# Kernel tuning notes

Measured on AMD Instinct MI355X. Metric: run time of the kernel, lower is better.

## Reference

```python
import jax, jax.numpy as jnp
import numpy as np
from jax import lax

STATE_LEN = 5
N_BASE = 4
C = N_BASE ** STATE_LEN          # 1024 CRF states
NZ = N_BASE + 1                  # 5 incoming transitions per state
FEAT = 320
KW = 19
STRIDE = 5
SCALE = 5.0


def _transition_idx():
    # bonito CTC_CRF.idx: predecessor state for each (state, transition) pair
    a = np.arange(C)
    idx = np.concatenate([a[:, None], np.repeat(a, N_BASE).reshape(N_BASE, -1).T], axis=1)
    return jnp.asarray(idx, dtype=jnp.int32)  # [C, NZ]


def setup_inputs() -> dict:
    key = jax.random.key(0)
    ks = jax.random.split(key, 5)
    x = jax.random.normal(ks[0], (32, 1, 4000), jnp.float32)
    conv_w = jax.random.normal(ks[1], (FEAT, 1, KW), jnp.float32) * 0.1
    conv_b = jax.random.normal(ks[2], (FEAT,), jnp.float32) * 0.1
    lin_w = jax.random.normal(ks[3], (FEAT, C * NZ), jnp.float32) * (1.0 / np.sqrt(FEAT))
    lin_b = jax.random.normal(ks[4], (C * NZ,), jnp.float32) * 0.1
    return {"x": x, "conv_w": conv_w, "conv_b": conv_b, "lin_w": lin_w, "lin_b": lin_b}


def _encoder(x, conv_w, conv_b, lin_w, lin_b):
    # x: [N, 1, L] -> strided conv -> [N, FEAT, T]
    y = lax.conv_general_dilated(x, conv_w, (STRIDE,), "SAME",
                                 dimension_numbers=("NCH", "OIH", "NCH"))
    y = jnp.tanh(y + conv_b[None, :, None])
    y = jnp.transpose(y, (2, 0, 1))  # [T, N, FEAT]
    # scaled-tanh CRF output head -> [T, N, C*NZ]
    return SCALE * jnp.tanh(jnp.einsum("tnf,fc->tnc", y, lin_w) + lin_b)


def _logZ(scores, idx):
    # log-semiring forward algorithm (alpha_0 = beta_T = 0)
    T, N, _ = scores.shape
    Ms = scores.reshape(T, N, C, NZ)
    alpha0 = jnp.zeros((N, C), scores.dtype)

    def step(alpha, Ms_t):  # Ms_t: [N, C, NZ], alpha: [N, C]
        return jax.nn.logsumexp(Ms_t + alpha[:, idx], axis=2), None

    alpha, _ = lax.scan(step, alpha0, Ms)
    return jax.nn.logsumexp(alpha, axis=1)  # [N]


def reference(x, conv_w, conv_b, lin_w, lin_b):
    idx = _transition_idx()
    scores = _encoder(x, conv_w, conv_b, lin_w, lin_b).astype(jnp.float32)  # [T, N, 5120]
    T = scores.shape[0]
    # GlobalNorm: scores - logZ / T, broadcast over time and channel dims
    return scores - _logZ(scores, idx)[:, None] / T
```

## Files before the change

### kernel.cpp

```cpp
#include <hip/hip_runtime.h>
#include <hip/hip_bf16.h>


typedef __attribute__((ext_vector_type(8))) short bf16x8;
typedef __attribute__((ext_vector_type(4))) float f32x4;

#define T_STEPS 800
#define NBATCH 32
#define FEAT 320
#define CNZ 5120
#define MROWS (T_STEPS * NBATCH)

__device__ __forceinline__ float fast_tanh(float x) {
    float e = exp2f(x * 2.8853900817779268f);
    return 1.0f - 2.0f * __builtin_amdgcn_rcpf(e + 1.0f);
}

__global__ __launch_bounds__(320) void conv_kernel(
    const float* __restrict__ x, const float* __restrict__ w,
    const float* __restrict__ b, __hip_bfloat16* __restrict__ y) {
    int m = blockIdx.x;
    int t = m >> 5, n = m & 31;
    int f = threadIdx.x;
    __shared__ float xs[19];
    int base = t * 5 - 7;
    if (f < 19) {
        int pos = base + f;
        xs[f] = (pos >= 0 && pos < 4000) ? x[n * 4000 + pos] : 0.0f;
    }
    __syncthreads();
    float acc = b[f];
#pragma unroll
    for (int k = 0; k < 19; ++k) acc = fmaf(xs[k], w[f * 19 + k], acc);
    y[(size_t)m * FEAT + f] = __float2bfloat16(fast_tanh(acc));
}

__global__ __launch_bounds__(256) void transpose_w(
    const float* __restrict__ W, __hip_bfloat16* __restrict__ Wt) {
    __shared__ float tile[64][65];
    int nb = blockIdx.x * 64, kb = blockIdx.y * 64;
    int tx = threadIdx.x & 63, ty = threadIdx.x >> 6;
#pragma unroll
    for (int r = 0; r < 64; r += 4)
        tile[ty + r][tx] = W[(size_t)(kb + ty + r) * CNZ + nb + tx];
    __syncthreads();
#pragma unroll
    for (int r = 0; r < 64; r += 4) {
        int nn = ty + r;
        Wt[(size_t)(nb + nn) * FEAT + kb + tx] = __float2bfloat16(tile[tx][nn]);
    }
}

#define GBM 128
#define GBN 128
#define GBK 64
#define LDK 72

__global__ __launch_bounds__(256) void gemm_kernel(
    const __hip_bfloat16* __restrict__ A,
    const __hip_bfloat16* __restrict__ Bt,
    const float* __restrict__ bias,
    float* __restrict__ out) {
    __shared__ __align__(16) short As[GBM * LDK];
    __shared__ __align__(16) short Bs[GBN * LDK];
    const int K = FEAT;
    int bm0 = blockIdx.x * GBM;
    int bn0 = blockIdx.y * GBN;
    int tid = threadIdx.x;
    int wave = tid >> 6, lane = tid & 63;
    int wm = (wave >> 1) * 64, wn = (wave & 1) * 64;
    int col = lane & 15, quad = lane >> 4;

    f32x4 acc[4][4];
#pragma unroll
    for (int i = 0; i < 4; ++i)
#pragma unroll
        for (int j = 0; j < 4; ++j) acc[i][j] = (f32x4){0.f, 0.f, 0.f, 0.f};

    for (int k0 = 0; k0 < K; k0 += GBK) {
#pragma unroll
        for (int p = 0; p < 4; ++p) {
            int i = p * 256 + tid;
            int row = i >> 3, cg = i & 7;
            *(int4*)&As[row * LDK + cg * 8] =
                *(const int4*)&A[(size_t)(bm0 + row) * K + k0 + cg * 8];
            *(int4*)&Bs[row * LDK + cg * 8] =
                *(const int4*)&Bt[(size_t)(bn0 + row) * K + k0 + cg * 8];
        }
        __syncthreads();
#pragma unroll
        for (int kk = 0; kk < GBK; kk += 32) {
            bf16x8 af[4], bfr[4];
#pragma unroll
            for (int i = 0; i < 4; ++i)
                af[i] = *(bf16x8*)&As[(wm + i * 16 + col) * LDK + kk + quad * 8];
#pragma unroll
            for (int j = 0; j < 4; ++j)
                bfr[j] = *(bf16x8*)&Bs[(wn + j * 16 + col) * LDK + kk + quad * 8];
#pragma unroll
            for (int i = 0; i < 4; ++i)
#pragma unroll
                for (int j = 0; j < 4; ++j)
                    acc[i][j] = __builtin_amdgcn_mfma_f32_16x16x32_bf16(
                        af[i], bfr[j], acc[i][j], 0, 0, 0);
        }
        __syncthreads();
    }
#pragma unroll
    for (int j = 0; j < 4; ++j) {
        int n_g = bn0 + wn + j * 16 + col;
        float bj = bias[n_g];
#pragma unroll
        for (int i = 0; i < 4; ++i) {
            int m_base = bm0 + wm + i * 16 + quad * 4;
#pragma unroll
            for (int r = 0; r < 4; ++r) {
                out[(size_t)(m_base + r) * CNZ + n_g] =
                    5.0f * fast_tanh(acc[i][j][r] + bj);
            }
        }
    }
}


__device__ __forceinline__ float lse5_2(float s0, float s1, float s2, float s3,
                                        float s4, float a0, float a1, float a2,
                                        float a3, float a4) {
    const float L2E = 1.4426950408889634f;
    float x0 = fmaf(s0, L2E, a0);
    float x1 = fmaf(s1, L2E, a1);
    float x2 = fmaf(s2, L2E, a2);
    float x3 = fmaf(s3, L2E, a3);
    float x4 = fmaf(s4, L2E, a4);
    float mx = fmaxf(fmaxf(fmaxf(x0, x1), fmaxf(x2, x3)), x4);
    float sum = __builtin_amdgcn_exp2f(x0 - mx) + __builtin_amdgcn_exp2f(x1 - mx) +
                __builtin_amdgcn_exp2f(x2 - mx) + __builtin_amdgcn_exp2f(x3 - mx) +
                __builtin_amdgcn_exp2f(x4 - mx);
    return __builtin_amdgcn_logf(sum) + mx;
}

#define LOADP(P, TT) do {                                                      \
    int tc_ = (TT) < T_STEPS ? (TT) : (T_STEPS - 1);                           \
    const float4* p4_ = (const float4*)(base + (size_t)tc_ * tstride);         \
    P[0] = p4_[0]; P[1] = p4_[1]; P[2] = p4_[2]; P[3] = p4_[3]; P[4] = p4_[4]; \
} while (0)

#define FSTEP(P, TT, cur, nxt) do {                                            \
    float s0_ = P[0].x, s1_ = P[0].y, s2_ = P[0].z, s3_ = P[0].w, s4_ = P[1].x;\
    float t0_ = P[1].y, t1_ = P[1].z, t2_ = P[1].w, t3_ = P[2].x, t4_ = P[2].y;\
    float u0_ = P[2].z, u1_ = P[2].w, u2_ = P[3].x, u3_ = P[3].y, u4_ = P[3].z;\
    float v0_ = P[3].w, v1_ = P[4].x, v2_ = P[4].y, v3_ = P[4].z, v4_ = P[4].w;\
    LOADP(P, TT);                                                              \
    float aq0_ = (cur)[tid], aq1_ = (cur)[tid + 256];                          \
    float aq2_ = (cur)[tid + 512], aq3_ = (cur)[tid + 768];                    \
    float4 ao_ = *(const float4*)&(cur)[4 * tid];                              \
    float4 r_;                                                                 \
    r_.x = lse5_2(s0_, s1_, s2_, s3_, s4_, ao_.x, aq0_, aq1_, aq2_, aq3_);     \
    r_.y = lse5_2(t0_, t1_, t2_, t3_, t4_, ao_.y, aq0_, aq1_, aq2_, aq3_);     \
    r_.z = lse5_2(u0_, u1_, u2_, u3_, u4_, ao_.z, aq0_, aq1_, aq2_, aq3_);     \
    r_.w = lse5_2(v0_, v1_, v2_, v3_, v4_, ao_.w, aq0_, aq1_, aq2_, aq3_);     \
    *(float4*)&(nxt)[4 * tid] = r_;                                            \
    __syncthreads();                                                           \
} while (0)

__global__ __launch_bounds__(256) void forward_kernel(
    const float* __restrict__ scores, float* __restrict__ corr) {
    __shared__ float A0[1024];
    __shared__ float A1[1024];
    const int tid = threadIdx.x;
    const int n = blockIdx.x;
    const float LN2 = 0.6931471805599453f;

    *(float4*)&A0[4 * tid] = (float4){0.f, 0.f, 0.f, 0.f};
    __syncthreads();

    const size_t tstride = (size_t)NBATCH * CNZ;
    const float* base = scores + (size_t)n * CNZ + tid * 20;

    float4 P0[5], P1[5], P2[5], P3[5];
    LOADP(P0, 0); LOADP(P1, 1); LOADP(P2, 2); LOADP(P3, 3);

    for (int t = 0; t < T_STEPS; t += 4) {
        FSTEP(P0, t + 4, A0, A1);
        FSTEP(P1, t + 5, A1, A0);
        FSTEP(P2, t + 6, A0, A1);
        FSTEP(P3, t + 7, A1, A0);
    }
    float4 v = *(const float4*)&A0[4 * tid];
    float pm = fmaxf(fmaxf(v.x, v.y), fmaxf(v.z, v.w));
    A1[tid] = pm;
    __syncthreads();
#pragma unroll
    for (int s = 128; s > 0; s >>= 1) {
        if (tid < s) A1[tid] = fmaxf(A1[tid], A1[tid + s]);
        __syncthreads();
    }
    float mx = A1[0];
    __syncthreads();
    float ps = __builtin_amdgcn_exp2f(v.x - mx) + __builtin_amdgcn_exp2f(v.y - mx) +
               __builtin_amdgcn_exp2f(v.z - mx) + __builtin_amdgcn_exp2f(v.w - mx);
    A1[tid] = ps;
    __syncthreads();
#pragma unroll
    for (int s = 128; s > 0; s >>= 1) {
        if (tid < s) A1[tid] += A1[tid + s];
        __syncthreads();
    }
    if (tid == 0)
        corr[n] = (__builtin_amdgcn_logf(A1[0]) + mx) * LN2 * (1.0f / (float)T_STEPS);
}

__global__ __launch_bounds__(256) void sub_kernel(
    float* __restrict__ out, const float* __restrict__ corr) {
    size_t i4 = (size_t)blockIdx.x * blockDim.x + threadIdx.x;
    float cc = corr[(i4 / (CNZ / 4)) & (NBATCH - 1)];
    float4* o4 = (float4*)out;
    float4 v = o4[i4];
    v.x -= cc; v.y -= cc; v.z -= cc; v.w -= cc;
    o4[i4] = v;
}

extern "C" void kernel_launch(void* const* d_in, const int* in_sizes, int n_in,
                              void* d_out, int out_size, void* d_ws, size_t ws_size,
                              hipStream_t stream) {
    const float* x      = (const float*)d_in[0];
    const float* conv_w = (const float*)d_in[1];
    const float* conv_b = (const float*)d_in[2];
    const float* lin_w  = (const float*)d_in[3];
    const float* lin_b  = (const float*)d_in[4];
    float* out = (float*)d_out;

    char* ws = (char*)d_ws;
    __hip_bfloat16* y  = (__hip_bfloat16*)ws;
    __hip_bfloat16* wt = (__hip_bfloat16*)(ws + 16384000);
    float* corr        = (float*)(ws + 16384000 + 3276800);

    conv_kernel<<<MROWS, 320, 0, stream>>>(x, conv_w, conv_b, y);
    transpose_w<<<dim3(CNZ / 64, FEAT / 64), 256, 0, stream>>>(lin_w, wt);
    gemm_kernel<<<dim3(MROWS / GBM, CNZ / GBN), 256, 0, stream>>>(y, wt, lin_b, out);
    forward_kernel<<<NBATCH, 256, 0, stream>>>(out, corr);
    sub_kernel<<<(out_size / 4) / 256, 256, 0, stream>>>(out, corr);
}
```

Before: 1.432 ms.

## Split CRF recursion into concurrent forward and backward halves with fp16 score copy

Replaces the single serial forward scan with a kernel that runs the forward pass over the first part of time and a backward pass over the rest in separate blocks. A combine kernel then joins alpha and beta to get logZ. This roughly halves the length of the serial dependency chain and doubles the number of busy blocks. The GEMM optionally writes an fp16 copy of the scores so the recursion reads half the bytes, which costs extra write traffic and some precision. The fp16 path is taken only when the workspace is large enough.

```diff
diff --git a/kernel.cpp b/kernel.cpp
--- a/kernel.cpp
+++ b/kernel.cpp
@@ -1,5 +1,7 @@
 #include <hip/hip_runtime.h>
 #include <hip/hip_bf16.h>
+#include <hip/hip_fp16.h>
+#include <type_traits>
 
 
 typedef __attribute__((ext_vector_type(8))) short bf16x8;
@@ -10,6 +12,8 @@
 #define FEAT 320
 #define CNZ 5120
 #define MROWS (T_STEPS * NBATCH)
+#define FSPLIT 480
+#define BSTEPS (T_STEPS - FSPLIT)
 
 __device__ __forceinline__ float fast_tanh(float x) {
     float e = exp2f(x * 2.8853900817779268f);
@@ -60,7 +64,8 @@
     const __hip_bfloat16* __restrict__ A,
     const __hip_bfloat16* __restrict__ Bt,
     const float* __restrict__ bias,
-    float* __restrict__ out) {
+    float* __restrict__ out,
+    __half* __restrict__ s16) {
     __shared__ __align__(16) short As[GBM * LDK];
     __shared__ __align__(16) short Bs[GBN * LDK];
     const int K = FEAT;
@@ -115,8 +120,10 @@
             int m_base = bm0 + wm + i * 16 + quad * 4;
 #pragma unroll
             for (int r = 0; r < 4; ++r) {
-                out[(size_t)(m_base + r) * CNZ + n_g] =
-                    5.0f * fast_tanh(acc[i][j][r] + bj);
+                size_t idx = (size_t)(m_base + r) * CNZ + n_g;
+                float v = 5.0f * fast_tanh(acc[i][j][r] + bj);
+                out[idx] = v;
+                if (s16) s16[idx] = __float2half(v);
             }
         }
     }
@@ -139,75 +146,141 @@
     return __builtin_amdgcn_logf(sum) + mx;
 }
 
-#define LOADP(P, TT) do {                                                      \
-    int tc_ = (TT) < T_STEPS ? (TT) : (T_STEPS - 1);                           \
-    const float4* p4_ = (const float4*)(base + (size_t)tc_ * tstride);         \
-    P[0] = p4_[0]; P[1] = p4_[1]; P[2] = p4_[2]; P[3] = p4_[3]; P[4] = p4_[4]; \
-} while (0)
-
-#define FSTEP(P, TT, cur, nxt) do {                                            \
-    float s0_ = P[0].x, s1_ = P[0].y, s2_ = P[0].z, s3_ = P[0].w, s4_ = P[1].x;\
-    float t0_ = P[1].y, t1_ = P[1].z, t2_ = P[1].w, t3_ = P[2].x, t4_ = P[2].y;\
-    float u0_ = P[2].z, u1_ = P[2].w, u2_ = P[3].x, u3_ = P[3].y, u4_ = P[3].z;\
-    float v0_ = P[3].w, v1_ = P[4].x, v2_ = P[4].y, v3_ = P[4].z, v4_ = P[4].w;\
-    LOADP(P, TT);                                                              \
-    float aq0_ = (cur)[tid], aq1_ = (cur)[tid + 256];                          \
-    float aq2_ = (cur)[tid + 512], aq3_ = (cur)[tid + 768];                    \
-    float4 ao_ = *(const float4*)&(cur)[4 * tid];                              \
-    float4 r_;                                                                 \
-    r_.x = lse5_2(s0_, s1_, s2_, s3_, s4_, ao_.x, aq0_, aq1_, aq2_, aq3_);     \
-    r_.y = lse5_2(t0_, t1_, t2_, t3_, t4_, ao_.y, aq0_, aq1_, aq2_, aq3_);     \
-    r_.z = lse5_2(u0_, u1_, u2_, u3_, u4_, ao_.z, aq0_, aq1_, aq2_, aq3_);     \
-    r_.w = lse5_2(v0_, v1_, v2_, v3_, v4_, ao_.w, aq0_, aq1_, aq2_, aq3_);     \
-    *(float4*)&(nxt)[4 * tid] = r_;                                            \
+__device__ __forceinline__ float cvh(ushort u) { __half h = *(__half*)&u; return __half2float(h); }
+__device__ __forceinline__ float cvh(float f) { return f; }
+
+template<bool FP16>
+__global__ __launch_bounds__(512) void fb_kernel(
+    const void* __restrict__ sc, float* __restrict__ alphaF,
+    float* __restrict__ betaB) {
+    __shared__ __align__(16) float A0[1024];
+    __shared__ __align__(16) float A1[1024];
+    const int tid = threadIdx.x;
+    const int n = blockIdx.x & 31;
+    const int dir = blockIdx.x >> 5;
+
+    *(float2*)&A0[2 * tid] = make_float2(0.f, 0.f);
+    __syncthreads();
+
+    const size_t row = (size_t)NBATCH * CNZ;
+
+    if (dir == 0) {
+        const int q = tid >> 1;
+        const uint* fbu = (const uint*)((const __half*)sc + (size_t)n * CNZ) +
+                          (size_t)tid * 5;
+        const float2* fbf = (const float2*)((const float*)sc + (size_t)n * CNZ +
+                          (size_t)tid * 10);
+
+#define LDF(P, TT) do { int tc_ = (TT) < FSPLIT ? (TT) : (FSPLIT - 1);         \
+    if constexpr (FP16) { const uint* pp_ = fbu + (size_t)tc_ * 81920;         \
+        P[0] = pp_[0]; P[1] = pp_[1]; P[2] = pp_[2]; P[3] = pp_[3]; P[4] = pp_[4]; } \
+    else { const float2* pp_ = fbf + (size_t)tc_ * 81920; float2* d_ = (float2*)P; \
+        d_[0] = pp_[0]; d_[1] = pp_[1]; d_[2] = pp_[2]; d_[3] = pp_[3]; d_[4] = pp_[4]; } \
+} while (0)
+
+#define UNP(P, s) do { if constexpr (FP16) {                                   \
+        float2 f0_ = __half22float2(*(__half2*)&P[0]);                         \
+        float2 f1_ = __half22float2(*(__half2*)&P[1]);                         \
+        float2 f2_ = __half22float2(*(__half2*)&P[2]);                         \
+        float2 f3_ = __half22float2(*(__half2*)&P[3]);                         \
+        float2 f4_ = __half22float2(*(__half2*)&P[4]);                         \
+        s[0]=f0_.x; s[1]=f0_.y; s[2]=f1_.x; s[3]=f1_.y; s[4]=f2_.x;            \
+        s[5]=f2_.y; s[6]=f3_.x; s[7]=f3_.y; s[8]=f4_.x; s[9]=f4_.y; }          \
+    else { const float* f_ = (const float*)P;                                  \
+        s[0]=f_[0]; s[1]=f_[1]; s[2]=f_[2]; s[3]=f_[3]; s[4]=f_[4];            \
+        s[5]=f_[5]; s[6]=f_[6]; s[7]=f_[7]; s[8]=f_[8]; s[9]=f_[9]; }          \
+} while (0)
+
+#define FSTEP(P, TT, cur, nxt) do { float s_[10]; UNP(P, s_); LDF(P, TT);      \
+    float aq0_ = (cur)[q], aq1_ = (cur)[q + 256];                              \
+    float aq2_ = (cur)[q + 512], aq3_ = (cur)[q + 768];                        \
+    float2 ao_ = *(const float2*)&(cur)[2 * tid];                              \
+    float r0_ = lse5_2(s_[0], s_[1], s_[2], s_[3], s_[4], ao_.x, aq0_, aq1_, aq2_, aq3_); \
+    float r1_ = lse5_2(s_[5], s_[6], s_[7], s_[8], s_[9], ao_.y, aq0_, aq1_, aq2_, aq3_); \
+    *(float2*)&(nxt)[2 * tid] = make_float2(r0_, r1_);                         \
     __syncthreads();                                                           \
 } while (0)
 
-__global__ __launch_bounds__(256) void forward_kernel(
-    const float* __restrict__ scores, float* __restrict__ corr) {
-    __shared__ float A0[1024];
-    __shared__ float A1[1024];
-    const int tid = threadIdx.x;
-    const int n = blockIdx.x;
-    const float LN2 = 0.6931471805599453f;
-
-    *(float4*)&A0[4 * tid] = (float4){0.f, 0.f, 0.f, 0.f};
-    __syncthreads();
-
-    const size_t tstride = (size_t)NBATCH * CNZ;
-    const float* base = scores + (size_t)n * CNZ + tid * 20;
-
-    float4 P0[5], P1[5], P2[5], P3[5];
-    LOADP(P0, 0); LOADP(P1, 1); LOADP(P2, 2); LOADP(P3, 3);
-
-    for (int t = 0; t < T_STEPS; t += 4) {
-        FSTEP(P0, t + 4, A0, A1);
-        FSTEP(P1, t + 5, A1, A0);
-        FSTEP(P2, t + 6, A0, A1);
-        FSTEP(P3, t + 7, A1, A0);
-    }
-    float4 v = *(const float4*)&A0[4 * tid];
-    float pm = fmaxf(fmaxf(v.x, v.y), fmaxf(v.z, v.w));
-    A1[tid] = pm;
+        uint P0[10], P1[10], P2[10], P3[10];
+        LDF(P0, 0); LDF(P1, 1); LDF(P2, 2); LDF(P3, 3);
+        for (int t = 0; t < FSPLIT; t += 4) {
+            FSTEP(P0, t + 4, A0, A1);
+            FSTEP(P1, t + 5, A1, A0);
+            FSTEP(P2, t + 6, A0, A1);
+            FSTEP(P3, t + 7, A1, A0);
+        }
+        *(float2*)&alphaF[(size_t)n * 1024 + 2 * tid] = *(const float2*)&A0[2 * tid];
+    } else {
+        using ET = std::conditional_t<FP16, ushort, float>;
+        const int p0 = 2 * tid;
+        const int g = p0 & 255;
+        const int hi = p0 >> 8;
+        const size_t o_self = (size_t)10 * tid;
+        const size_t gb = (size_t)20 * g + 1 + hi;
+        const ET* bb = (const ET*)sc + (size_t)n * CNZ;
+        const int sbase = (8 * tid) & 1023;
+
+#define LDB(E, KK) do { int kc_ = (KK) < BSTEPS ? (KK) : (BSTEPS - 1);         \
+    const ET* pb_ = bb + (size_t)(T_STEPS - 1 - kc_) * row;                    \
+    E[0] = pb_[o_self];      E[1] = pb_[gb];       E[2] = pb_[gb + 5];         \
+    E[3] = pb_[gb + 10];     E[4] = pb_[gb + 15];  E[5] = pb_[o_self + 5];     \
+    E[6] = pb_[gb + 20];     E[7] = pb_[gb + 25];  E[8] = pb_[gb + 30];        \
+    E[9] = pb_[gb + 35];                                                       \
+} while (0)
+
+#define BSTEP(E, KK, cur, nxt) do { float s_[10];                              \
+    s_[0]=cvh(E[0]); s_[1]=cvh(E[1]); s_[2]=cvh(E[2]); s_[3]=cvh(E[3]);        \
+    s_[4]=cvh(E[4]); s_[5]=cvh(E[5]); s_[6]=cvh(E[6]); s_[7]=cvh(E[7]);        \
+    s_[8]=cvh(E[8]); s_[9]=cvh(E[9]); LDB(E, KK);                              \
+    float2 bs_ = *(const float2*)&(cur)[2 * tid];                              \
+    float4 b0_ = *(const float4*)&(cur)[sbase];                                \
+    float4 b1_ = *(const float4*)&(cur)[sbase + 4];                            \
+    float r0_ = lse5_2(s_[0], s_[1], s_[2], s_[3], s_[4], bs_.x, b0_.x, b0_.y, b0_.z, b0_.w); \
+    float r1_ = lse5_2(s_[5], s_[6], s_[7], s_[8], s_[9], bs_.y, b1_.x, b1_.y, b1_.z, b1_.w); \
+    *(float2*)&(nxt)[2 * tid] = make_float2(r0_, r1_);                         \
+    __syncthreads();                                                           \
+} while (0)
+
+        ET E0[10], E1[10], E2[10], E3[10];
+        LDB(E0, 0); LDB(E1, 1); LDB(E2, 2); LDB(E3, 3);
+        for (int k = 0; k < BSTEPS; k += 4) {
+            BSTEP(E0, k + 4, A0, A1);
+            BSTEP(E1, k + 5, A1, A0);
+            BSTEP(E2, k + 6, A0, A1);
+            BSTEP(E3, k + 7, A1, A0);
+        }
+        *(float2*)&betaB[(size_t)n * 1024 + 2 * tid] = *(const float2*)&A0[2 * tid];
+    }
+}
+
+__global__ __launch_bounds__(256) void combine_kernel(
+    const float* __restrict__ aF, const float* __restrict__ bB,
+    float* __restrict__ corr) {
+    __shared__ float R[256];
+    int n = blockIdx.x, tid = threadIdx.x;
+    float4 a = *(const float4*)&aF[(size_t)n * 1024 + 4 * tid];
+    float4 b = *(const float4*)&bB[(size_t)n * 1024 + 4 * tid];
+    float x0 = a.x + b.x, x1 = a.y + b.y, x2 = a.z + b.z, x3 = a.w + b.w;
+    float m = fmaxf(fmaxf(x0, x1), fmaxf(x2, x3));
+    R[tid] = m;
     __syncthreads();
 #pragma unroll
     for (int s = 128; s > 0; s >>= 1) {
-        if (tid < s) A1[tid] = fmaxf(A1[tid], A1[tid + s]);
+        if (tid < s) R[tid] = fmaxf(R[tid], R[tid + s]);
         __syncthreads();
     }
-    float mx = A1[0];
-    __syncthreads();
-    float ps = __builtin_amdgcn_exp2f(v.x - mx) + __builtin_amdgcn_exp2f(v.y - mx) +
-               __builtin_amdgcn_exp2f(v.z - mx) + __builtin_amdgcn_exp2f(v.w - mx);
-    A1[tid] = ps;
+    float mx = R[0];
+    __syncthreads();
+    float sm = exp2f(x0 - mx) + exp2f(x1 - mx) + exp2f(x2 - mx) + exp2f(x3 - mx);
+    R[tid] = sm;
     __syncthreads();
 #pragma unroll
     for (int s = 128; s > 0; s >>= 1) {
-        if (tid < s) A1[tid] += A1[tid + s];
+        if (tid < s) R[tid] += R[tid + s];
         __syncthreads();
     }
     if (tid == 0)
-        corr[n] = (__builtin_amdgcn_logf(A1[0]) + mx) * LN2 * (1.0f / (float)T_STEPS);
+        corr[n] = (log2f(R[0]) + mx) * 0.6931471805599453f * (1.0f / (float)T_STEPS);
 }
 
 __global__ __launch_bounds__(256) void sub_kernel(
@@ -230,14 +303,30 @@
     const float* lin_b  = (const float*)d_in[4];
     float* out = (float*)d_out;
 
+    const size_t Y_OFF    = 0;
+    const size_t WT_OFF   = 16384000;
+    const size_t CORR_OFF = 19660800;
+    const size_t AF_OFF   = 19661056;
+    const size_t BB_OFF   = 19792128;
+    const size_t S16_OFF  = 19923200;
+    const size_t NEED16   = S16_OFF + (size_t)MROWS * CNZ * 2;
+
     char* ws = (char*)d_ws;
-    __hip_bfloat16* y  = (__hip_bfloat16*)ws;
-    __hip_bfloat16* wt = (__hip_bfloat16*)(ws + 16384000);
-    float* corr        = (float*)(ws + 16384000 + 3276800);
+    __hip_bfloat16* y  = (__hip_bfloat16*)(ws + Y_OFF);
+    __hip_bfloat16* wt = (__hip_bfloat16*)(ws + WT_OFF);
+    float* corr = (float*)(ws + CORR_OFF);
+    float* aF   = (float*)(ws + AF_OFF);
+    float* bB   = (float*)(ws + BB_OFF);
+    bool fp16_path = ws_size >= NEED16;
+    __half* s16 = fp16_path ? (__half*)(ws + S16_OFF) : nullptr;
 
     conv_kernel<<<MROWS, 320, 0, stream>>>(x, conv_w, conv_b, y);
     transpose_w<<<dim3(CNZ / 64, FEAT / 64), 256, 0, stream>>>(lin_w, wt);
-    gemm_kernel<<<dim3(MROWS / GBM, CNZ / GBN), 256, 0, stream>>>(y, wt, lin_b, out);
-    forward_kernel<<<NBATCH, 256, 0, stream>>>(out, corr);
+    gemm_kernel<<<dim3(MROWS / GBM, CNZ / GBN), 256, 0, stream>>>(y, wt, lin_b, out, s16);
+    if (fp16_path)
+        fb_kernel<true><<<64, 512, 0, stream>>>(s16, aF, bB);
+    else
+        fb_kernel<false><<<64, 512, 0, stream>>>(out, aF, bB);
+    combine_kernel<<<NBATCH, 256, 0, stream>>>(aF, bB, corr);
     sub_kernel<<<(out_size / 4) / 256, 256, 0, stream>>>(out, corr);
 }
```

New measurement: 1.416 ms. Within noise of the previous version (-1.2%).
